# Kernel optimization log

Hardware: AMD Instinct MI355X
Metric: run time of the kernel (lower is better)

Reference implementation:

```python
import jax, jax.numpy as jnp
import numpy as np

EPS = 1e-6
NEG_CLAMP = -20.0


def setup_inputs() -> dict:
    key = jax.random.key(0)
    kq, kk, kv = jax.random.split(key, 3)
    B, L, H, E = 8, 4096, 16, 64
    queries = jax.random.normal(kq, (B, L, H, E), dtype=jnp.float32)
    keys = jax.random.normal(kk, (B, L, H, E), dtype=jnp.float32)
    values = jax.random.normal(kv, (B, L, H, E), dtype=jnp.float32)
    delta1 = jnp.zeros((), dtype=jnp.float32)  # nn.Parameter(torch.tensor(0.0))
    return {"queries": queries, "keys": keys, "values": values, "delta1": delta1}


def reference(queries, keys, values, delta1):
    # [B,L,H,E] -> [B,H,L,E]
    q = jnp.swapaxes(queries, 1, 2)
    k = jnp.swapaxes(keys, 1, 2)
    v = jnp.swapaxes(values, 1, 2)

    # mapping_fun == 'softmax_learn': clamp negatives to -20, temperature = softplus(delta1)
    temp = jax.nn.softplus(delta1)
    q = jax.nn.softmax(jnp.where(q < 0, NEG_CLAMP, q) / temp, axis=-1)
    k = jax.nn.softmax(jnp.where(k < 0, NEG_CLAMP, k) / temp, axis=-1)

    # kv = sum_l k[...,l,d] v[...,l,e]  -> [B,H,E,E]
    kv = jnp.einsum('bhld,bhle->bhde', k, v)
    # z_l = 1 / (q_l . sum_l k_l)
    k_sum = k.sum(axis=2)  # [B,H,E]
    z = 1.0 / (jnp.einsum('bhld,bhd->bhl', q, k_sum) + EPS)
    # output [B,L,H,E]
    out = jnp.einsum('bhle,bhed,bhl->blhd', q, kv, z)
    return out
```

## Files before the change

### kernel.cpp

```cpp
#include <hip/hip_runtime.h>

#define L_DIM 4096
#define H_DIM 16
#define E_DIM 64
#define BH 128
#define ROWSTRIDE 1024

#define P1_CHUNK 512
#define P2_CHUNK 512

__device__ __forceinline__ float inv_softplus_temp(const float* delta1) {
  return 1.0f / log1pf(__expf(delta1[0]));
}

__global__ __launch_bounds__(256) void p1_kv(
    const float* __restrict__ Kp, const float* __restrict__ Vp,
    const float* __restrict__ delta1,
    float* __restrict__ ws_kv, float* __restrict__ ws_ksum) {
  const int t = threadIdx.x;
  const int bh = blockIdx.y;
  const int b = bh >> 4, h = bh & 15;
  const int lane = t & 63;
  const int w = t >> 6;
  const float inv_temp = inv_softplus_temp(delta1);
  const size_t base = ((size_t)b * L_DIM * H_DIM + h) * E_DIM;
  const int l0 = blockIdx.x * P1_CHUNK;

  __shared__ float sk[16][64];
  __shared__ float sv[16][64];

  const int rsub = lane >> 4;
  const int equad = (lane & 15) << 2;
  const int srow = (w << 2) | rsub;

  const int d0 = (t >> 4) << 2;
  const int e0 = (t & 15) << 2;

  float acc[4][4];
  float ks[4];
#pragma unroll
  for (int i = 0; i < 4; ++i) {
    ks[i] = 0.f;
#pragma unroll
    for (int j = 0; j < 4; ++j) acc[i][j] = 0.f;
  }

  for (int it = 0; it < P1_CHUNK / 16; ++it) {
    const int l = l0 + it * 16 + srow;
    const float4 k4 = *(const float4*)(Kp + base + (size_t)l * ROWSTRIDE + equad);
    const float4 v4 = *(const float4*)(Vp + base + (size_t)l * ROWSTRIDE + equad);
    float ex = __expf((k4.x < 0.f ? -20.f : k4.x) * inv_temp);
    float ey = __expf((k4.y < 0.f ? -20.f : k4.y) * inv_temp);
    float ez = __expf((k4.z < 0.f ? -20.f : k4.z) * inv_temp);
    float ew = __expf((k4.w < 0.f ? -20.f : k4.w) * inv_temp);
    float s = ex + ey + ez + ew;
    s += __shfl_xor(s, 1);
    s += __shfl_xor(s, 2);
    s += __shfl_xor(s, 4);
    s += __shfl_xor(s, 8);
    const float rs = __builtin_amdgcn_rcpf(s);

    __syncthreads();
    *(float4*)&sk[srow][equad] = make_float4(ex * rs, ey * rs, ez * rs, ew * rs);
    *(float4*)&sv[srow][equad] = v4;
    __syncthreads();

#pragma unroll
    for (int rr = 0; rr < 16; ++rr) {
      const float4 kk = *(const float4*)&sk[rr][d0];
      const float4 vv = *(const float4*)&sv[rr][e0];
      const float ka[4] = {kk.x, kk.y, kk.z, kk.w};
      const float va[4] = {vv.x, vv.y, vv.z, vv.w};
#pragma unroll
      for (int i = 0; i < 4; ++i)
#pragma unroll
        for (int j = 0; j < 4; ++j)
          acc[i][j] = fmaf(ka[i], va[j], acc[i][j]);
      if (e0 == 0) {
        ks[0] += ka[0]; ks[1] += ka[1]; ks[2] += ka[2]; ks[3] += ka[3];
      }
    }
  }

  float* kvdst = ws_kv + (size_t)bh * 4096;
#pragma unroll
  for (int i = 0; i < 4; ++i)
#pragma unroll
    for (int j = 0; j < 4; ++j)
      atomicAdd(&kvdst[(d0 + i) * 64 + (e0 + j)], acc[i][j]);
  if (e0 == 0) {
#pragma unroll
    for (int i = 0; i < 4; ++i)
      atomicAdd(&ws_ksum[bh * 64 + d0 + i], ks[i]);
  }
}

__global__ __launch_bounds__(256) void p2_out(
    const float* __restrict__ Qp, const float* __restrict__ delta1,
    const float* __restrict__ ws_kv, const float* __restrict__ ws_ksum,
    float* __restrict__ outp) {
  const int t = threadIdx.x;
  const int bh = blockIdx.y;
  const int b = bh >> 4, h = bh & 15;
  const int lane = t & 63;
  const int w = t >> 6;
  const float inv_temp = inv_softplus_temp(delta1);
  const size_t base = ((size_t)b * L_DIM * H_DIM + h) * E_DIM;
  const int l0 = blockIdx.x * P2_CHUNK;

  const int rsub = lane >> 4;
  const int equad = (lane & 15) << 2;

  float kvcol[64];
#pragma unroll
  for (int e = 0; e < 64; ++e)
    kvcol[e] = ws_kv[(size_t)bh * 4096 + e * 64 + lane];

  const float4 ks4 = *(const float4*)&ws_ksum[bh * 64 + equad];

  __shared__ float sWT[4][64][4];

  for (int it = 0; it < P2_CHUNK / 16; ++it) {
    const int l = l0 + it * 16 + (w << 2) + rsub;
    const float4 q4 = *(const float4*)(Qp + base + (size_t)l * ROWSTRIDE + equad);
    float ex = __expf((q4.x < 0.f ? -20.f : q4.x) * inv_temp);
    float ey = __expf((q4.y < 0.f ? -20.f : q4.y) * inv_temp);
    float ez = __expf((q4.z < 0.f ? -20.f : q4.z) * inv_temp);
    float ew = __expf((q4.w < 0.f ? -20.f : q4.w) * inv_temp);
    float sE = ex + ey + ez + ew;
    float sD = ex * ks4.x + ey * ks4.y + ez * ks4.z + ew * ks4.w;
    sE += __shfl_xor(sE, 1); sD += __shfl_xor(sD, 1);
    sE += __shfl_xor(sE, 2); sD += __shfl_xor(sD, 2);
    sE += __shfl_xor(sE, 4); sD += __shfl_xor(sD, 4);
    sE += __shfl_xor(sE, 8); sD += __shfl_xor(sD, 8);
    const float scale = __builtin_amdgcn_rcpf(sD + 1e-6f * sE);

    __syncthreads();
    sWT[w][equad + 0][rsub] = ex * scale;
    sWT[w][equad + 1][rsub] = ey * scale;
    sWT[w][equad + 2][rsub] = ez * scale;
    sWT[w][equad + 3][rsub] = ew * scale;
    __syncthreads();

    float a0 = 0.f, a1 = 0.f, a2 = 0.f, a3 = 0.f;
#pragma unroll
    for (int e = 0; e < 64; ++e) {
      const float4 wv = *(const float4*)&sWT[w][e][0];
      const float kve = kvcol[e];
      a0 = fmaf(wv.x, kve, a0);
      a1 = fmaf(wv.y, kve, a1);
      a2 = fmaf(wv.z, kve, a2);
      a3 = fmaf(wv.w, kve, a3);
    }

    const size_t ob = base + (size_t)(l0 + it * 16 + (w << 2)) * ROWSTRIDE + lane;
    outp[ob] = a0;
    outp[ob + ROWSTRIDE] = a1;
    outp[ob + 2 * (size_t)ROWSTRIDE] = a2;
    outp[ob + 3 * (size_t)ROWSTRIDE] = a3;
  }
}

extern "C" void kernel_launch(void* const* d_in, const int* in_sizes, int n_in,
                              void* d_out, int out_size, void* d_ws, size_t ws_size,
                              hipStream_t stream) {
  (void)in_sizes; (void)n_in; (void)out_size; (void)ws_size;
  const float* Q = (const float*)d_in[0];
  const float* K = (const float*)d_in[1];
  const float* V = (const float*)d_in[2];
  const float* delta1 = (const float*)d_in[3];
  float* out = (float*)d_out;

  float* ws_kv = (float*)d_ws;
  float* ws_ksum = ws_kv + (size_t)BH * 4096;
  const size_t zero_bytes = ((size_t)BH * 4096 + (size_t)BH * 64) * sizeof(float);
  hipMemsetAsync(d_ws, 0, zero_bytes, stream);

  dim3 blk(256);
  dim3 g1(L_DIM / P1_CHUNK, BH);
  p1_kv<<<g1, blk, 0, stream>>>(K, V, delta1, ws_kv, ws_ksum);
  dim3 g2(L_DIM / P2_CHUNK, BH);
  p2_out<<<g2, blk, 0, stream>>>(Q, delta1, ws_kv, ws_ksum, out);
}
```

Measured before the change: 503.0 us.

## Give each wavefront its own L slice, drop block barriers, prefetch next rows

Each wavefront now handles a contiguous quarter of the block's sequence chunk with private LDS staging. This replaces per-iteration __syncthreads with a wave-local lgkmcnt wait. In the KV pass each lane accumulates an 8x8 outer-product tile, and the four wave partials are reduced through LDS before the global atomics, which adds 16 KB of shared memory and raises register pressure. Both kernels also software-prefetch the next K/V or Q rows into registers to overlap global loads with compute.

New measurement: 697.8 us. +38.7%, slower.

```diff
diff --git a/kernel.cpp b/kernel.cpp
--- a/kernel.cpp
+++ b/kernel.cpp
@@ -13,7 +13,11 @@
   return 1.0f / log1pf(__expf(delta1[0]));
 }
 
-__global__ __launch_bounds__(256) void p1_kv(
+__device__ __forceinline__ void lds_fence() {
+  asm volatile("s_waitcnt lgkmcnt(0)" ::: "memory");
+}
+
+__global__ __launch_bounds__(256, 4) void p1_kv(
     const float* __restrict__ Kp, const float* __restrict__ Vp,
     const float* __restrict__ delta1,
     float* __restrict__ ws_kv, float* __restrict__ ws_ksum) {
@@ -24,31 +28,36 @@
   const int w = t >> 6;
   const float inv_temp = inv_softplus_temp(delta1);
   const size_t base = ((size_t)b * L_DIM * H_DIM + h) * E_DIM;
-  const int l0 = blockIdx.x * P1_CHUNK;
-
-  __shared__ float sk[16][64];
-  __shared__ float sv[16][64];
+  const int l0 = blockIdx.x * P1_CHUNK + w * (P1_CHUNK / 4);
 
   const int rsub = lane >> 4;
   const int equad = (lane & 15) << 2;
-  const int srow = (w << 2) | rsub;
-
-  const int d0 = (t >> 4) << 2;
-  const int e0 = (t & 15) << 2;
-
-  float acc[4][4];
-  float ks[4];
-#pragma unroll
-  for (int i = 0; i < 4; ++i) {
-    ks[i] = 0.f;
-#pragma unroll
-    for (int j = 0; j < 4; ++j) acc[i][j] = 0.f;
-  }
-
-  for (int it = 0; it < P1_CHUNK / 16; ++it) {
-    const int l = l0 + it * 16 + srow;
-    const float4 k4 = *(const float4*)(Kp + base + (size_t)l * ROWSTRIDE + equad);
-    const float4 v4 = *(const float4*)(Vp + base + (size_t)l * ROWSTRIDE + equad);
+  const int d0 = (lane >> 3) << 3;
+  const int e0 = (lane & 7) << 3;
+
+  __shared__ float sk[4][4][64];
+  __shared__ float sv[4][4][64];
+  __shared__ float red[4096];
+
+  float acc[8][8];
+#pragma unroll
+  for (int i = 0; i < 8; ++i)
+#pragma unroll
+    for (int j = 0; j < 8; ++j) acc[i][j] = 0.f;
+  float ksk[4] = {0.f, 0.f, 0.f, 0.f};
+
+  const int NIT = (P1_CHUNK / 4) / 4;
+  const float* kp = Kp + base + (size_t)(l0 + rsub) * ROWSTRIDE + equad;
+  const float* vp = Vp + base + (size_t)(l0 + rsub) * ROWSTRIDE + equad;
+
+  float4 k4 = *(const float4*)kp;
+  float4 v4 = *(const float4*)vp;
+
+  for (int it = 0; it < NIT; ++it) {
+    const int pit = (it + 1 < NIT) ? it + 1 : it;
+    const float4 nk4 = *(const float4*)(kp + (size_t)pit * (4 * ROWSTRIDE));
+    const float4 nv4 = *(const float4*)(vp + (size_t)pit * (4 * ROWSTRIDE));
+
     float ex = __expf((k4.x < 0.f ? -20.f : k4.x) * inv_temp);
     float ey = __expf((k4.y < 0.f ? -20.f : k4.y) * inv_temp);
     float ez = __expf((k4.z < 0.f ? -20.f : k4.z) * inv_temp);
@@ -59,43 +68,69 @@
     s += __shfl_xor(s, 4);
     s += __shfl_xor(s, 8);
     const float rs = __builtin_amdgcn_rcpf(s);
-
-    __syncthreads();
-    *(float4*)&sk[srow][equad] = make_float4(ex * rs, ey * rs, ez * rs, ew * rs);
-    *(float4*)&sv[srow][equad] = v4;
-    __syncthreads();
-
-#pragma unroll
-    for (int rr = 0; rr < 16; ++rr) {
-      const float4 kk = *(const float4*)&sk[rr][d0];
-      const float4 vv = *(const float4*)&sv[rr][e0];
-      const float ka[4] = {kk.x, kk.y, kk.z, kk.w};
-      const float va[4] = {vv.x, vv.y, vv.z, vv.w};
-#pragma unroll
-      for (int i = 0; i < 4; ++i)
-#pragma unroll
-        for (int j = 0; j < 4; ++j)
+    ex *= rs; ey *= rs; ez *= rs; ew *= rs;
+    ksk[0] += ex; ksk[1] += ey; ksk[2] += ez; ksk[3] += ew;
+
+    *(float4*)&sk[w][rsub][equad] = make_float4(ex, ey, ez, ew);
+    *(float4*)&sv[w][rsub][equad] = v4;
+    lds_fence();
+
+#pragma unroll
+    for (int r = 0; r < 4; ++r) {
+      const float4 ka0 = *(const float4*)&sk[w][r][d0];
+      const float4 ka1 = *(const float4*)&sk[w][r][d0 + 4];
+      const float4 va0 = *(const float4*)&sv[w][r][e0];
+      const float4 va1 = *(const float4*)&sv[w][r][e0 + 4];
+      const float ka[8] = {ka0.x, ka0.y, ka0.z, ka0.w, ka1.x, ka1.y, ka1.z, ka1.w};
+      const float va[8] = {va0.x, va0.y, va0.z, va0.w, va1.x, va1.y, va1.z, va1.w};
+#pragma unroll
+      for (int i = 0; i < 8; ++i)
+#pragma unroll
+        for (int j = 0; j < 8; ++j)
           acc[i][j] = fmaf(ka[i], va[j], acc[i][j]);
-      if (e0 == 0) {
-        ks[0] += ka[0]; ks[1] += ka[1]; ks[2] += ka[2]; ks[3] += ka[3];
+    }
+    k4 = nk4;
+    v4 = nv4;
+  }
+
+#pragma unroll 1
+  for (int pass = 0; pass < 4; ++pass) {
+    if (w == pass) {
+#pragma unroll
+      for (int i = 0; i < 8; ++i) {
+#pragma unroll
+        for (int jq = 0; jq < 2; ++jq) {
+          float4* p = (float4*)&red[(d0 + i) * 64 + e0 + jq * 4];
+          float4 c = (pass == 0) ? make_float4(0.f, 0.f, 0.f, 0.f) : *p;
+          c.x += acc[i][jq * 4 + 0];
+          c.y += acc[i][jq * 4 + 1];
+          c.z += acc[i][jq * 4 + 2];
+          c.w += acc[i][jq * 4 + 3];
+          *p = c;
+        }
       }
     }
+    __syncthreads();
   }
 
   float* kvdst = ws_kv + (size_t)bh * 4096;
 #pragma unroll
-  for (int i = 0; i < 4; ++i)
-#pragma unroll
-    for (int j = 0; j < 4; ++j)
-      atomicAdd(&kvdst[(d0 + i) * 64 + (e0 + j)], acc[i][j]);
-  if (e0 == 0) {
-#pragma unroll
-    for (int i = 0; i < 4; ++i)
-      atomicAdd(&ws_ksum[bh * 64 + d0 + i], ks[i]);
-  }
-}
-
-__global__ __launch_bounds__(256) void p2_out(
+  for (int rr = 0; rr < 16; ++rr)
+    atomicAdd(&kvdst[rr * 256 + t], red[rr * 256 + t]);
+
+  ksk[0] += __shfl_xor(ksk[0], 16); ksk[0] += __shfl_xor(ksk[0], 32);
+  ksk[1] += __shfl_xor(ksk[1], 16); ksk[1] += __shfl_xor(ksk[1], 32);
+  ksk[2] += __shfl_xor(ksk[2], 16); ksk[2] += __shfl_xor(ksk[2], 32);
+  ksk[3] += __shfl_xor(ksk[3], 16); ksk[3] += __shfl_xor(ksk[3], 32);
+  if (lane < 16) {
+    atomicAdd(&ws_ksum[bh * 64 + equad + 0], ksk[0]);
+    atomicAdd(&ws_ksum[bh * 64 + equad + 1], ksk[1]);
+    atomicAdd(&ws_ksum[bh * 64 + equad + 2], ksk[2]);
+    atomicAdd(&ws_ksum[bh * 64 + equad + 3], ksk[3]);
+  }
+}
+
+__global__ __launch_bounds__(256, 4) void p2_out(
     const float* __restrict__ Qp, const float* __restrict__ delta1,
     const float* __restrict__ ws_kv, const float* __restrict__ ws_ksum,
     float* __restrict__ outp) {
@@ -106,7 +141,7 @@
   const int w = t >> 6;
   const float inv_temp = inv_softplus_temp(delta1);
   const size_t base = ((size_t)b * L_DIM * H_DIM + h) * E_DIM;
-  const int l0 = blockIdx.x * P2_CHUNK;
+  const int l0 = blockIdx.x * P2_CHUNK + w * (P2_CHUNK / 4);
 
   const int rsub = lane >> 4;
   const int equad = (lane & 15) << 2;
@@ -120,9 +155,15 @@
 
   __shared__ float sWT[4][64][4];
 
-  for (int it = 0; it < P2_CHUNK / 16; ++it) {
-    const int l = l0 + it * 16 + (w << 2) + rsub;
-    const float4 q4 = *(const float4*)(Qp + base + (size_t)l * ROWSTRIDE + equad);
+  const int NIT = (P2_CHUNK / 4) / 4;
+  const float* qp = Qp + base + (size_t)(l0 + rsub) * ROWSTRIDE + equad;
+  float* op0 = outp + base + (size_t)l0 * ROWSTRIDE + lane;
+
+  float4 q4 = *(const float4*)qp;
+  for (int it = 0; it < NIT; ++it) {
+    const int pit = (it + 1 < NIT) ? it + 1 : it;
+    const float4 nq4 = *(const float4*)(qp + (size_t)pit * (4 * ROWSTRIDE));
+
     float ex = __expf((q4.x < 0.f ? -20.f : q4.x) * inv_temp);
     float ey = __expf((q4.y < 0.f ? -20.f : q4.y) * inv_temp);
     float ez = __expf((q4.z < 0.f ? -20.f : q4.z) * inv_temp);
@@ -135,12 +176,11 @@
     sE += __shfl_xor(sE, 8); sD += __shfl_xor(sD, 8);
     const float scale = __builtin_amdgcn_rcpf(sD + 1e-6f * sE);
 
-    __syncthreads();
     sWT[w][equad + 0][rsub] = ex * scale;
     sWT[w][equad + 1][rsub] = ey * scale;
     sWT[w][equad + 2][rsub] = ez * scale;
     sWT[w][equad + 3][rsub] = ew * scale;
-    __syncthreads();
+    lds_fence();
 
     float a0 = 0.f, a1 = 0.f, a2 = 0.f, a3 = 0.f;
 #pragma unroll
@@ -153,11 +193,12 @@
       a3 = fmaf(wv.w, kve, a3);
     }
 
-    const size_t ob = base + (size_t)(l0 + it * 16 + (w << 2)) * ROWSTRIDE + lane;
-    outp[ob] = a0;
-    outp[ob + ROWSTRIDE] = a1;
-    outp[ob + 2 * (size_t)ROWSTRIDE] = a2;
-    outp[ob + 3 * (size_t)ROWSTRIDE] = a3;
+    float* op = op0 + (size_t)it * (4 * ROWSTRIDE);
+    op[0] = a0;
+    op[ROWSTRIDE] = a1;
+    op[2 * (size_t)ROWSTRIDE] = a2;
+    op[3 * (size_t)ROWSTRIDE] = a3;
+    q4 = nq4;
   }
 }
 
```
